# Kernel optimization log

Hardware: AMD Instinct MI355X
Metric: run time of the kernel (lower is better)

The kernel has to match this reference:

```python
import jax, jax.numpy as jnp
import numpy as np

WS = 7      # window_size
NH = 12     # num_heads
SHIFT = 3   # shift_size

def _rel_pos_index(ws):
    coords = np.stack(np.meshgrid(np.arange(ws), np.arange(ws), indexing='ij')).reshape(2, -1)
    rel = (coords[:, :, None] - coords[:, None, :]).transpose(1, 2, 0)  # [N,N,2]
    rel[..., 0] += ws - 1
    rel[..., 1] += ws - 1
    rel[..., 0] *= 2 * ws - 1
    return jnp.asarray(rel.sum(-1))  # [N,N] int

REL_IDX = _rel_pos_index(WS)

def _ln(x, g, b, eps=1e-5):
    m = x.mean(-1, keepdims=True)
    v = ((x - m) ** 2).mean(-1, keepdims=True)
    return (x - m) / jnp.sqrt(v + eps) * g + b

def setup_inputs() -> dict:
    key = jax.random.key(0)
    ks = jax.random.split(key, 10)
    B, H, W, C = 16, 56, 56, 384
    Dff = 4 * C
    s = 0.02
    return {
        'x': jax.random.normal(ks[0], (B, H * W, C), jnp.float32),
        'norm1_g': jnp.ones((C,), jnp.float32),
        'norm1_b': jnp.zeros((C,), jnp.float32),
        'qkv_w': jax.random.normal(ks[1], (3 * C, C), jnp.float32) * s,
        'qkv_b': jax.random.normal(ks[2], (3 * C,), jnp.float32) * s,
        'proj_w': jax.random.normal(ks[3], (C, C), jnp.float32) * s,
        'proj_b': jax.random.normal(ks[4], (C,), jnp.float32) * s,
        'rpb_table': jax.random.normal(ks[5], ((2 * WS - 1) ** 2, NH), jnp.float32) * s,
        'norm2_g': jnp.ones((C,), jnp.float32),
        'norm2_b': jnp.zeros((C,), jnp.float32),
        'mlp_w1': jax.random.normal(ks[6], (Dff, C), jnp.float32) * s,
        'mlp_b1': jax.random.normal(ks[7], (Dff,), jnp.float32) * s,
        'mlp_w2': jax.random.normal(ks[8], (C, Dff), jnp.float32) * s,
        'mlp_b2': jax.random.normal(ks[9], (C,), jnp.float32) * s,
        'H': H,
        'W': W,
    }

def reference(x, norm1_g, norm1_b, qkv_w, qkv_b, proj_w, proj_b, rpb_table,
              norm2_g, norm2_b, mlp_w1, mlp_b1, mlp_w2, mlp_b2, H, W):
    B, L, C = x.shape
    # --- norm1 + shift + window partition ---
    h = _ln(x, norm1_g, norm1_b).reshape(B, H, W, C)
    h = jnp.roll(h, (-SHIFT, -SHIFT), axis=(1, 2))
    nh, nw = H // WS, W // WS
    xw = h.reshape(B, nh, WS, nw, WS, C).transpose(0, 1, 3, 2, 4, 5).reshape(-1, WS * WS, C)
    # --- window attention with relative position bias ---
    Bw, N, _ = xw.shape
    hd = C // NH
    qkv = (xw @ qkv_w.T + qkv_b).reshape(Bw, N, 3, NH, hd).transpose(2, 0, 3, 1, 4)
    q, k, v = qkv[0] * (hd ** -0.5), qkv[1], qkv[2]  # [Bw,NH,N,hd]
    attn = jnp.einsum('bhnd,bhmd->bhnm', q, k)
    bias = rpb_table[REL_IDX.reshape(-1)].reshape(N, N, NH).transpose(2, 0, 1)  # [NH,N,N]
    attn = jax.nn.softmax(attn + bias[None], axis=-1)
    o = jnp.einsum('bhnm,bhmd->bhnd', attn, v).transpose(0, 2, 1, 3).reshape(Bw, N, C)
    o = o @ proj_w.T + proj_b
    # --- window reverse + unshift + residual ---
    o = o.reshape(B, nh, nw, WS, WS, C).transpose(0, 1, 3, 2, 4, 5).reshape(B, H, W, C)
    o = jnp.roll(o, (SHIFT, SHIFT), axis=(1, 2)).reshape(B, L, C)
    x = x + o
    # --- MLP ---
    h = _ln(x, norm2_g, norm2_b)
    h = jax.nn.gelu(h @ mlp_w1.T + mlp_b1, approximate=False) @ mlp_w2.T + mlp_b2
    return x + h
```

## Files before the change

kernel.cpp:

```cpp
#include <hip/hip_runtime.h>

typedef unsigned short ushort_t;
typedef unsigned int uint32;
typedef __attribute__((ext_vector_type(8))) short short8;
typedef __attribute__((ext_vector_type(4))) float floatx4;

static __device__ __forceinline__ ushort_t f2bf(float f) {
    union { float f; unsigned int u; } c; c.f = f;
    unsigned int u = c.u;
    return (ushort_t)((u + 0x7FFFu + ((u >> 16) & 1u)) >> 16);
}

static __device__ __forceinline__ int swz_off(int row, int slot16) {
    return row * 64 + (((slot16 ^ (row & 7)) & 7) << 3);
}

__global__ __launch_bounds__(256) void cvt_weights(
    const float* __restrict__ w0, const float* __restrict__ w1,
    const float* __restrict__ w2, const float* __restrict__ w3,
    ushort_t* __restrict__ o0, ushort_t* __restrict__ o1,
    ushort_t* __restrict__ o2, ushort_t* __restrict__ o3)
{
    int i = blockIdx.x * 256 + threadIdx.x;
    if (i < 442368) o0[i] = f2bf(w0[i]);
    if (i < 147456) o1[i] = f2bf(w1[i]);
    if (i < 589824) o2[i] = f2bf(w2[i]);
    if (i < 589824) o3[i] = f2bf(w3[i]);
}

__global__ __launch_bounds__(256) void build_bias(
    const float* __restrict__ rpb, float* __restrict__ biasM)
{
    int idx = blockIdx.x * 256 + threadIdx.x;
    int h = idx >> 12, q = (idx >> 6) & 63, j = idx & 63;
    float v = 0.f;
    if (q < 49 && j < 49) {
        int pi = q / 7, pj = q - pi * 7;
        int qi = j / 7, qj = j - qi * 7;
        v = rpb[((pi - qi + 6) * 13 + (pj - qj + 6)) * 12 + h];
    }
    biasM[idx] = v;
}

template<bool WPART>
__global__ __launch_bounds__(256) void ln_kernel(
    const float* __restrict__ x, const float* __restrict__ g,
    const float* __restrict__ b, ushort_t* __restrict__ out)
{
    int wave = threadIdx.x >> 6, lane = threadIdx.x & 63;
    int tkn = blockIdx.x * 4 + wave;
    const float* src;
    if (WPART) {
        int w = tkn / 49, n = tkn - w * 49;
        int bb = w >> 6, wrem = w & 63;
        int wi = wrem >> 3, wj = wrem & 7;
        int pi = n / 7, pj = n - pi * 7;
        int si = wi * 7 + pi + 3; if (si >= 56) si -= 56;
        int sj = wj * 7 + pj + 3; if (sj >= 56) sj -= 56;
        src = x + ((size_t)bb * 3136 + si * 56 + sj) * 384;
    } else {
        src = x + (size_t)tkn * 384;
    }
    float v[6];
    float s = 0.f, sq = 0.f;
#pragma unroll
    for (int it = 0; it < 3; ++it) {
        float2 t = *(const float2*)(src + it * 128 + lane * 2);
        v[it * 2] = t.x; v[it * 2 + 1] = t.y;
        s += t.x + t.y; sq += t.x * t.x + t.y * t.y;
    }
#pragma unroll
    for (int off = 32; off; off >>= 1) {
        s += __shfl_xor(s, off, 64);
        sq += __shfl_xor(sq, off, 64);
    }
    float mean = s * (1.f / 384.f);
    float rstd = rsqrtf(sq * (1.f / 384.f) - mean * mean + 1e-5f);
    ushort_t* dst = out + (size_t)tkn * 384;
#pragma unroll
    for (int it = 0; it < 3; ++it) {
        int c = it * 128 + lane * 2;
        float2 gg = *(const float2*)(g + c);
        float2 bb2 = *(const float2*)(b + c);
        float y0 = (v[it * 2] - mean) * rstd * gg.x + bb2.x;
        float y1 = (v[it * 2 + 1] - mean) * rstd * gg.y + bb2.y;
        uint32 pack = ((uint32)f2bf(y0)) | (((uint32)f2bf(y1)) << 16);
        *(uint32*)(dst + c) = pack;
    }
}

template<int EPI>
__global__ __launch_bounds__(256, 2) void gemm_bt(
    const ushort_t* __restrict__ A, const ushort_t* __restrict__ Bw,
    const float* __restrict__ bias, void* __restrict__ out,
    const float* __restrict__ resid, int M, int N, int K)
{
    __shared__ __align__(16) ushort_t As[2][128 * 64];
    __shared__ __align__(16) ushort_t Bs[2][128 * 64];
    int tid = threadIdx.x;

    int nwg = gridDim.x;
    int orig = blockIdx.x;
    int xcd = orig & 7, lid = orig >> 3;
    int q8 = nwg >> 3, r8 = nwg & 7;
    int swz = (xcd < r8 ? xcd * (q8 + 1) : r8 * (q8 + 1) + (xcd - r8) * q8) + lid;
    int bnT = N >> 7;
    int bm = swz / bnT, bn = swz - bm * bnT;

    int wv = tid >> 6, lane = tid & 63;
    int wr = wv >> 1, wc = wv & 1;
    int quad = lane >> 4, l15 = lane & 15;
    int r0 = tid >> 3, s0 = tid & 7;

    floatx4 acc[4][4];
#pragma unroll
    for (int mi = 0; mi < 4; ++mi)
#pragma unroll
        for (int ni = 0; ni < 4; ++ni)
            acc[mi][ni] = (floatx4){0.f, 0.f, 0.f, 0.f};

    const ushort_t* Ar0 = A + (size_t)(bm * 128 + r0) * K + s0 * 8;
    const ushort_t* Ar1 = Ar0 + (size_t)32 * K;
    const ushort_t* Ar2 = Ar0 + (size_t)64 * K;
    const ushort_t* Ar3 = Ar0 + (size_t)96 * K;
    const ushort_t* Br0 = Bw + (size_t)(bn * 128 + r0) * K + s0 * 8;
    const ushort_t* Br1 = Br0 + (size_t)32 * K;
    const ushort_t* Br2 = Br0 + (size_t)64 * K;
    const ushort_t* Br3 = Br0 + (size_t)96 * K;

    int w0 = swz_off(r0, s0), w1 = swz_off(r0 + 32, s0);
    int w2 = swz_off(r0 + 64, s0), w3 = swz_off(r0 + 96, s0);

    int nK = K >> 6;
    uint4 ra0, ra1, ra2, ra3, rb0, rb1, rb2, rb3;

    ra0 = *(const uint4*)Ar0;  ra1 = *(const uint4*)Ar1;
    ra2 = *(const uint4*)Ar2;  ra3 = *(const uint4*)Ar3;
    rb0 = *(const uint4*)Br0;  rb1 = *(const uint4*)Br1;
    rb2 = *(const uint4*)Br2;  rb3 = *(const uint4*)Br3;
    *(uint4*)&As[0][w0] = ra0;  *(uint4*)&As[0][w1] = ra1;
    *(uint4*)&As[0][w2] = ra2;  *(uint4*)&As[0][w3] = ra3;
    *(uint4*)&Bs[0][w0] = rb0;  *(uint4*)&Bs[0][w1] = rb1;
    *(uint4*)&Bs[0][w2] = rb2;  *(uint4*)&Bs[0][w3] = rb3;

    int cur = 0;
    for (int kt = 0; kt < nK; ++kt) {
        __syncthreads();
        if (kt + 1 < nK) {
            int k0 = (kt + 1) << 6;
            ra0 = *(const uint4*)(Ar0 + k0);  ra1 = *(const uint4*)(Ar1 + k0);
            ra2 = *(const uint4*)(Ar2 + k0);  ra3 = *(const uint4*)(Ar3 + k0);
            rb0 = *(const uint4*)(Br0 + k0);  rb1 = *(const uint4*)(Br1 + k0);
            rb2 = *(const uint4*)(Br2 + k0);  rb3 = *(const uint4*)(Br3 + k0);
        }
#pragma unroll
        for (int kk = 0; kk < 64; kk += 32) {
            short8 af[4], bfr[4];
#pragma unroll
            for (int mi = 0; mi < 4; ++mi)
                af[mi] = *(const short8*)&As[cur][swz_off(wr * 64 + mi * 16 + l15, (kk >> 3) + quad)];
#pragma unroll
            for (int ni = 0; ni < 4; ++ni)
                bfr[ni] = *(const short8*)&Bs[cur][swz_off(wc * 64 + ni * 16 + l15, (kk >> 3) + quad)];
#pragma unroll
            for (int mi = 0; mi < 4; ++mi)
#pragma unroll
                for (int ni = 0; ni < 4; ++ni)
                    acc[mi][ni] = __builtin_amdgcn_mfma_f32_16x16x32_bf16(
                        af[mi], bfr[ni], acc[mi][ni], 0, 0, 0);
        }
        if (kt + 1 < nK) {
            *(uint4*)&As[cur ^ 1][w0] = ra0;  *(uint4*)&As[cur ^ 1][w1] = ra1;
            *(uint4*)&As[cur ^ 1][w2] = ra2;  *(uint4*)&As[cur ^ 1][w3] = ra3;
            *(uint4*)&Bs[cur ^ 1][w0] = rb0;  *(uint4*)&Bs[cur ^ 1][w1] = rb1;
            *(uint4*)&Bs[cur ^ 1][w2] = rb2;  *(uint4*)&Bs[cur ^ 1][w3] = rb3;
        }
        cur ^= 1;
    }

#pragma unroll
    for (int mi = 0; mi < 4; ++mi) {
#pragma unroll
        for (int ni = 0; ni < 4; ++ni) {
            int gn = bn * 128 + wc * 64 + ni * 16 + l15;
            float bv = bias[gn];
#pragma unroll
            for (int r = 0; r < 4; ++r) {
                int gm = bm * 128 + wr * 64 + mi * 16 + quad * 4 + r;
                float v = acc[mi][ni][r] + bv;
                if (EPI == 0) {
                    if (gn < 384) v *= 0.17677669529663689f;
                    ((ushort_t*)out)[(size_t)gm * N + gn] = f2bf(v);
                } else if (EPI == 1) {
                    v = 0.5f * v * (1.f + erff(v * 0.70710678118654752f));
                    ((ushort_t*)out)[(size_t)gm * N + gn] = f2bf(v);
                } else if (EPI == 2) {
                    int wdx = gm / 49, n = gm - wdx * 49;
                    int b = wdx >> 6, wrem = wdx & 63;
                    int wi = wrem >> 3, wj = wrem & 7;
                    int pi = n / 7, pj = n - pi * 7;
                    int i = wi * 7 + pi + 3; if (i >= 56) i -= 56;
                    int j = wj * 7 + pj + 3; if (j >= 56) j -= 56;
                    size_t dst = ((size_t)b * 3136 + i * 56 + j) * 384 + gn;
                    ((float*)out)[dst] = resid[dst] + v;
                } else {
                    size_t dst = (size_t)gm * 384 + gn;
                    ((float*)out)[dst] = resid[dst] + v;
                }
            }
        }
    }
}

__global__ __launch_bounds__(256) void attn_kernel(
    const ushort_t* __restrict__ qkv,
    const float* __restrict__ biasM,
    ushort_t* __restrict__ O)
{
    __shared__ __align__(16) ushort_t Pl[4][64][72];
    __shared__ __align__(16) ushort_t Vt[4][32][72];
    int wave = threadIdx.x >> 6;
    int lane = threadIdx.x & 63;
    int id = blockIdx.x * 4 + wave;
    int w = id / 12, h = id % 12;
    int quad = lane >> 4, l15 = lane & 15;
    ushort_t (*P)[72] = Pl[wave];
    ushort_t (*V)[72] = Vt[wave];

    for (int i = lane; i < 32 * 16; i += 64) {
        int d = i >> 4, j = 48 + (i & 15);
        V[d][j] = 0;
    }
    for (int idx = lane; idx < 49 * 4; idx += 64) {
        int j = idx >> 2, seg = idx & 3;
        const ushort_t* src = qkv + (size_t)(w * 49 + j) * 1152 + 768 + h * 32 + seg * 8;
        uint4 u = *(const uint4*)src;
        const ushort_t* tmp = (const ushort_t*)&u;
#pragma unroll
        for (int t = 0; t < 8; ++t) V[seg * 8 + t][j] = tmp[t];
    }

    short8 aQ[4], bK[4];
#pragma unroll
    for (int t = 0; t < 4; ++t) {
        int row = t * 16 + l15; if (row > 48) row = 48;
        aQ[t] = *(const short8*)(qkv + (size_t)(w * 49 + row) * 1152 + h * 32 + quad * 8);
        bK[t] = *(const short8*)(qkv + (size_t)(w * 49 + row) * 1152 + 384 + h * 32 + quad * 8);
    }
    floatx4 S[4][4];
    floatx4 z4 = (floatx4){0.f, 0.f, 0.f, 0.f};
#pragma unroll
    for (int mt = 0; mt < 4; ++mt)
#pragma unroll
        for (int nt = 0; nt < 4; ++nt)
            S[mt][nt] = __builtin_amdgcn_mfma_f32_16x16x32_bf16(aQ[mt], bK[nt], z4, 0, 0, 0);

    const float* bh = biasM + h * 4096;
#pragma unroll
    for (int mt = 0; mt < 4; ++mt) {
#pragma unroll
        for (int r = 0; r < 4; ++r) {
            int q = mt * 16 + quad * 4 + r;
            float mx = -1e30f;
#pragma unroll
            for (int nt = 0; nt < 4; ++nt) {
                int j = nt * 16 + l15;
                float sv = S[mt][nt][r] + bh[q * 64 + j];
                if (j >= 49) sv = -1e30f;
                S[mt][nt][r] = sv;
                mx = fmaxf(mx, sv);
            }
#pragma unroll
            for (int off = 1; off < 16; off <<= 1) mx = fmaxf(mx, __shfl_xor(mx, off, 64));
            float sum = 0.f;
#pragma unroll
            for (int nt = 0; nt < 4; ++nt) {
                int j = nt * 16 + l15;
                float p = __expf(S[mt][nt][r] - mx);
                if (j >= 49) p = 0.f;
                S[mt][nt][r] = p;
                sum += p;
            }
#pragma unroll
            for (int off = 1; off < 16; off <<= 1) sum += __shfl_xor(sum, off, 64);
            float inv = 1.f / sum;
#pragma unroll
            for (int nt = 0; nt < 4; ++nt) {
                int j = nt * 16 + l15;
                P[q][j] = f2bf(S[mt][nt][r] * inv);
            }
        }
    }
    __syncthreads();

    short8 aV[2][2];
#pragma unroll
    for (int mt = 0; mt < 2; ++mt)
#pragma unroll
        for (int kt = 0; kt < 2; ++kt)
            aV[mt][kt] = *(const short8*)&V[mt * 16 + l15][kt * 32 + quad * 8];
    floatx4 Oc[2][4];
#pragma unroll
    for (int mt = 0; mt < 2; ++mt)
#pragma unroll
        for (int nt = 0; nt < 4; ++nt)
            Oc[mt][nt] = z4;
#pragma unroll
    for (int nt = 0; nt < 4; ++nt) {
#pragma unroll
        for (int kt = 0; kt < 2; ++kt) {
            short8 bP = *(const short8*)&P[nt * 16 + l15][kt * 32 + quad * 8];
#pragma unroll
            for (int mt = 0; mt < 2; ++mt)
                Oc[mt][nt] = __builtin_amdgcn_mfma_f32_16x16x32_bf16(
                    aV[mt][kt], bP, Oc[mt][nt], 0, 0, 0);
        }
    }
#pragma unroll
    for (int nt = 0; nt < 4; ++nt) {
        int query = nt * 16 + l15;
        if (query < 49) {
#pragma unroll
            for (int mt = 0; mt < 2; ++mt) {
                ushort4 pk;
                pk.x = f2bf(Oc[mt][nt][0]);
                pk.y = f2bf(Oc[mt][nt][1]);
                pk.z = f2bf(Oc[mt][nt][2]);
                pk.w = f2bf(Oc[mt][nt][3]);
                *(ushort4*)(O + (size_t)(w * 49 + query) * 384 + h * 32 + mt * 16 + quad * 4) = pk;
            }
        }
    }
}

extern "C" void kernel_launch(void* const* d_in, const int* in_sizes, int n_in,
                              void* d_out, int out_size, void* d_ws, size_t ws_size,
                              hipStream_t stream) {
    const float* x      = (const float*)d_in[0];
    const float* n1g    = (const float*)d_in[1];
    const float* n1b    = (const float*)d_in[2];
    const float* qkv_w  = (const float*)d_in[3];
    const float* qkv_b  = (const float*)d_in[4];
    const float* proj_w = (const float*)d_in[5];
    const float* proj_b = (const float*)d_in[6];
    const float* rpb    = (const float*)d_in[7];
    const float* n2g    = (const float*)d_in[8];
    const float* n2b    = (const float*)d_in[9];
    const float* w1     = (const float*)d_in[10];
    const float* b1     = (const float*)d_in[11];
    const float* w2     = (const float*)d_in[12];
    const float* b2     = (const float*)d_in[13];
    float* out = (float*)d_out;
    char* ws = (char*)d_ws;

    ushort_t* qkvbuf = (ushort_t*)ws;
    ushort_t* bufA   = (ushort_t*)(ws + 115605504);
    ushort_t* wq     = (ushort_t*)(ws + 154140672);
    ushort_t* wp     = wq + 442368;
    ushort_t* wm1    = wp + 147456;
    ushort_t* wm2    = wm1 + 589824;
    float* biasM     = (float*)(ws + 154140672 + 3538944);

    cvt_weights<<<2304, 256, 0, stream>>>(qkv_w, proj_w, w1, w2, wq, wp, wm1, wm2);
    build_bias<<<192, 256, 0, stream>>>(rpb, biasM);

    ln_kernel<true><<<12544, 256, 0, stream>>>(x, n1g, n1b, bufA);
    gemm_bt<0><<<3528, 256, 0, stream>>>(bufA, wq, qkv_b, qkvbuf, nullptr, 50176, 1152, 384);
    attn_kernel<<<3072, 256, 0, stream>>>(qkvbuf, biasM, bufA);
    gemm_bt<2><<<1176, 256, 0, stream>>>(bufA, wp, proj_b, out, x, 50176, 384, 384);
    ln_kernel<false><<<12544, 256, 0, stream>>>(out, n2g, n2b, bufA);
    for (int half = 0; half < 2; ++half) {
        size_t mo = (size_t)half * 25088;
        gemm_bt<1><<<2352, 256, 0, stream>>>(bufA + mo * 384, wm1, b1, qkvbuf, nullptr, 25088, 1536, 384);
        gemm_bt<3><<<588, 256, 0, stream>>>(qkvbuf, wm2, b2, out + mo * 384, out + mo * 384, 25088, 384, 1536);
    }
}
```

Before: 591.8 us.

## Deepen GEMM global-to-LDS prefetch to two register stages with 2x unrolled loop

The bf16 MFMA GEMM main loop is unrolled by two, and two register sets of global loads are kept in flight, so each tile is fetched two K-steps ahead instead of one. LDS buffer indices become compile-time constants, which removes the dynamic `cur` indexing. The intent is to hide global memory latency better behind the MFMA work. The cost is extra VGPR pressure from 32 more registers, which may lower occupancy. The code also now assumes the K-tile count is even.

```diff
diff --git a/kernel.cpp b/kernel.cpp
--- a/kernel.cpp
+++ b/kernel.cpp
@@ -131,52 +131,61 @@
     int w0 = swz_off(r0, s0), w1 = swz_off(r0 + 32, s0);
     int w2 = swz_off(r0 + 64, s0), w3 = swz_off(r0 + 96, s0);
 
+#define GLOAD(a0,a1,a2,a3,b0,b1,b2,b3,k0) \
+    a0 = *(const uint4*)(Ar0 + (k0)); a1 = *(const uint4*)(Ar1 + (k0)); \
+    a2 = *(const uint4*)(Ar2 + (k0)); a3 = *(const uint4*)(Ar3 + (k0)); \
+    b0 = *(const uint4*)(Br0 + (k0)); b1 = *(const uint4*)(Br1 + (k0)); \
+    b2 = *(const uint4*)(Br2 + (k0)); b3 = *(const uint4*)(Br3 + (k0));
+
+#define SWRITE(buf,a0,a1,a2,a3,b0,b1,b2,b3) \
+    *(uint4*)&As[buf][w0] = a0; *(uint4*)&As[buf][w1] = a1; \
+    *(uint4*)&As[buf][w2] = a2; *(uint4*)&As[buf][w3] = a3; \
+    *(uint4*)&Bs[buf][w0] = b0; *(uint4*)&Bs[buf][w1] = b1; \
+    *(uint4*)&Bs[buf][w2] = b2; *(uint4*)&Bs[buf][w3] = b3;
+
+#define COMPUTE(buf) \
+    _Pragma("unroll") \
+    for (int kk = 0; kk < 64; kk += 32) { \
+        short8 af[4], bfr[4]; \
+        _Pragma("unroll") \
+        for (int mi = 0; mi < 4; ++mi) \
+            af[mi] = *(const short8*)&As[buf][swz_off(wr * 64 + mi * 16 + l15, (kk >> 3) + quad)]; \
+        _Pragma("unroll") \
+        for (int ni = 0; ni < 4; ++ni) \
+            bfr[ni] = *(const short8*)&Bs[buf][swz_off(wc * 64 + ni * 16 + l15, (kk >> 3) + quad)]; \
+        _Pragma("unroll") \
+        for (int mi = 0; mi < 4; ++mi) \
+            _Pragma("unroll") \
+            for (int ni = 0; ni < 4; ++ni) \
+                acc[mi][ni] = __builtin_amdgcn_mfma_f32_16x16x32_bf16( \
+                    af[mi], bfr[ni], acc[mi][ni], 0, 0, 0); \
+    }
+
     int nK = K >> 6;
-    uint4 ra0, ra1, ra2, ra3, rb0, rb1, rb2, rb3;
-
-    ra0 = *(const uint4*)Ar0;  ra1 = *(const uint4*)Ar1;
-    ra2 = *(const uint4*)Ar2;  ra3 = *(const uint4*)Ar3;
-    rb0 = *(const uint4*)Br0;  rb1 = *(const uint4*)Br1;
-    rb2 = *(const uint4*)Br2;  rb3 = *(const uint4*)Br3;
-    *(uint4*)&As[0][w0] = ra0;  *(uint4*)&As[0][w1] = ra1;
-    *(uint4*)&As[0][w2] = ra2;  *(uint4*)&As[0][w3] = ra3;
-    *(uint4*)&Bs[0][w0] = rb0;  *(uint4*)&Bs[0][w1] = rb1;
-    *(uint4*)&Bs[0][w2] = rb2;  *(uint4*)&Bs[0][w3] = rb3;
-
-    int cur = 0;
-    for (int kt = 0; kt < nK; ++kt) {
+    uint4 pa0, pa1, pa2, pa3, pb0, pb1, pb2, pb3;
+    uint4 qa0, qa1, qa2, qa3, qb0, qb1, qb2, qb3;
+
+    GLOAD(pa0, pa1, pa2, pa3, pb0, pb1, pb2, pb3, 0);
+    GLOAD(qa0, qa1, qa2, qa3, qb0, qb1, qb2, qb3, 64);
+    SWRITE(0, pa0, pa1, pa2, pa3, pb0, pb1, pb2, pb3);
+    if (nK > 2) { GLOAD(pa0, pa1, pa2, pa3, pb0, pb1, pb2, pb3, 128); }
+    __syncthreads();
+
+    for (int kt = 0; kt < nK; kt += 2) {
+        COMPUTE(0);
+        SWRITE(1, qa0, qa1, qa2, qa3, qb0, qb1, qb2, qb3);
+        if (kt + 3 < nK) { int k0 = (kt + 3) << 6; GLOAD(qa0, qa1, qa2, qa3, qb0, qb1, qb2, qb3, k0); }
         __syncthreads();
-        if (kt + 1 < nK) {
-            int k0 = (kt + 1) << 6;
-            ra0 = *(const uint4*)(Ar0 + k0);  ra1 = *(const uint4*)(Ar1 + k0);
-            ra2 = *(const uint4*)(Ar2 + k0);  ra3 = *(const uint4*)(Ar3 + k0);
-            rb0 = *(const uint4*)(Br0 + k0);  rb1 = *(const uint4*)(Br1 + k0);
-            rb2 = *(const uint4*)(Br2 + k0);  rb3 = *(const uint4*)(Br3 + k0);
-        }
-#pragma unroll
-        for (int kk = 0; kk < 64; kk += 32) {
-            short8 af[4], bfr[4];
-#pragma unroll
-            for (int mi = 0; mi < 4; ++mi)
-                af[mi] = *(const short8*)&As[cur][swz_off(wr * 64 + mi * 16 + l15, (kk >> 3) + quad)];
-#pragma unroll
-            for (int ni = 0; ni < 4; ++ni)
-                bfr[ni] = *(const short8*)&Bs[cur][swz_off(wc * 64 + ni * 16 + l15, (kk >> 3) + quad)];
-#pragma unroll
-            for (int mi = 0; mi < 4; ++mi)
-#pragma unroll
-                for (int ni = 0; ni < 4; ++ni)
-                    acc[mi][ni] = __builtin_amdgcn_mfma_f32_16x16x32_bf16(
-                        af[mi], bfr[ni], acc[mi][ni], 0, 0, 0);
-        }
-        if (kt + 1 < nK) {
-            *(uint4*)&As[cur ^ 1][w0] = ra0;  *(uint4*)&As[cur ^ 1][w1] = ra1;
-            *(uint4*)&As[cur ^ 1][w2] = ra2;  *(uint4*)&As[cur ^ 1][w3] = ra3;
-            *(uint4*)&Bs[cur ^ 1][w0] = rb0;  *(uint4*)&Bs[cur ^ 1][w1] = rb1;
-            *(uint4*)&Bs[cur ^ 1][w2] = rb2;  *(uint4*)&Bs[cur ^ 1][w3] = rb3;
-        }
-        cur ^= 1;
-    }
+        COMPUTE(1);
+        if (kt + 2 < nK) {
+            SWRITE(0, pa0, pa1, pa2, pa3, pb0, pb1, pb2, pb3);
+            if (kt + 4 < nK) { int k0 = (kt + 4) << 6; GLOAD(pa0, pa1, pa2, pa3, pb0, pb1, pb2, pb3, k0); }
+            __syncthreads();
+        }
+    }
+#undef GLOAD
+#undef SWRITE
+#undef COMPUTE
 
 #pragma unroll
     for (int mi = 0; mi < 4; ++mi) {
```

After: 579.1 us. 1.02x faster.
